# Performance work log

Hardware: AMD Instinct MI355X
Metric: run time of the kernel (lower is better)

Reference implementation:

```python
import jax, jax.numpy as jnp
import numpy as np

N_SCALES = 11
N_TAPS = 4
D4 = [0.4829629131445341, 0.8365163037378079, 0.2241438680420134, -0.1294095225512604]
B, N, D, H = 4, 2048, 1024, 16
HD = D // H  # 64


def setup_inputs() -> dict:
    key = jax.random.key(0)
    ks = jax.random.split(key, 8)
    s = 0.02
    return {
        "x": jax.random.normal(ks[0], (B, N, D), jnp.float32),
        "W_qkv": jax.random.normal(ks[1], (3 * D, D), jnp.float32) * s,
        "b_qkv": jnp.zeros((3 * D,), jnp.float32),
        "W_out": jax.random.normal(ks[2], (D, D), jnp.float32) * s,
        "b_out": jnp.zeros((D,), jnp.float32),
        "W_gate": jax.random.normal(ks[3], (D, D), jnp.float32) * s,
        "b_gate": jnp.full((D,), 2.0, jnp.float32),  # nn.init.constant_(gate bias, 2.0)
        "scale_gain": jax.random.normal(ks[4], (N_SCALES, H), jnp.float32) * 0.1,
        "W_qscale": jax.random.normal(ks[5], (N_SCALES, HD), jnp.float32) * 0.01,
        "identity_bypass": jnp.full((H,), -4.0, jnp.float32),
        "pos_bias": jax.random.normal(ks[6], (N_SCALES * N_TAPS, H), jnp.float32) * 0.01,
    }


def reference(x, W_qkv, b_qkv, W_out, b_out, W_gate, b_gate, scale_gain, W_qscale, identity_bypass, pos_bias):
    # qkv projection and head split -> [B,H,N,HD]
    qkv = x @ W_qkv.T + b_qkv
    q, k, v = jnp.split(qkv, 3, axis=-1)
    to_heads = lambda t: t.reshape(B, N, H, HD).transpose(0, 2, 1, 3)
    q, k, v = to_heads(q), to_heads(k), to_heads(v)

    # Q-conditioned per-scale gains: [B,H,N,n_scales]
    q_offset = jnp.einsum('bhnd,sd->bhns', q, W_qscale)
    prior = scale_gain.T[None, :, None, :]  # [1,H,1,S]
    gains = jax.nn.softmax(q_offset + prior, axis=-1)

    out = jnp.zeros((B, H, N, HD), q.dtype)
    z = jnp.zeros((B, H, N, 1), q.dtype)
    tap_idx = 0
    for j in range(N_SCALES):  # fixed small structural loop (44 taps total)
        d = 1 << j
        g_j = gains[..., j][..., None]  # [B,H,N,1]
        for tau, h_coef in enumerate(D4):
            offset = d * tau
            bias_jt = pos_bias[tap_idx].reshape(1, H, 1, 1)
            tap_idx += 1
            if offset != 0 and offset >= N:
                continue
            if offset == 0:
                k_s, v_s = k, v
            else:
                pad = jnp.zeros((B, H, offset, HD), k.dtype)
                k_s = jnp.concatenate([pad, k[:, :, :N - offset, :]], axis=2)
                v_s = jnp.concatenate([pad, v[:, :, :N - offset, :]], axis=2)
            qk_feat = jax.nn.elu(jnp.sum(q * k_s, -1, keepdims=True) + bias_jt) + 1.0
            out = out + (g_j * h_coef) * qk_feat * v_s
            z = z + g_j * abs(h_coef) * qk_feat

    # identity bypass (offset-0 local term)
    bypass = jax.nn.softplus(identity_bypass).reshape(1, H, 1, 1)
    local_ft = jax.nn.elu(jnp.sum(q * k, -1, keepdims=True)) + 1.0
    out = out + bypass * local_ft * v
    z = z + bypass * local_ft
    out = out / (z + 1e-06)

    gathered = out.transpose(0, 2, 1, 3).reshape(B, N, D)
    gate = jax.nn.sigmoid(x @ W_gate.T + b_gate)
    return (gathered * gate) @ W_out.T + b_out  # dropout p: eval mode -> identity
```

## Files before the change

kernel.cpp:

```cpp
#include <hip/hip_runtime.h>
#include <hip/hip_bf16.h>

#define PB 4
#define PN 2048
#define PD 1024
#define PH 16
#define PHD 64
#define NSC 11

typedef __attribute__((ext_vector_type(8))) short short8;
typedef __attribute__((ext_vector_type(4))) float floatx4;

#define AS1 __attribute__((address_space(1)))
#define AS3 __attribute__((address_space(3)))

static __device__ __forceinline__ unsigned short bf16bits(float f) {
    __hip_bfloat16 h = __float2bfloat16(f);
    return __builtin_bit_cast(unsigned short, h);
}

__global__ void cast_f32_to_bf16_v4(const float4* __restrict__ in,
                                    ushort4* __restrict__ out, int n4) {
    int i = blockIdx.x * blockDim.x + threadIdx.x;
    if (i < n4) {
        float4 v = in[i];
        ushort4 o;
        o.x = bf16bits(v.x);
        o.y = bf16bits(v.y);
        o.z = bf16bits(v.z);
        o.w = bf16bits(v.w);
        out[i] = o;
    }
}

#define GBM 128
#define GBN 128
#define GBK 64

template <int EPI>
__global__ __launch_bounds__(256) void gemm_bt128(
    const __hip_bfloat16* __restrict__ A,
    const __hip_bfloat16* __restrict__ Bm,
    const float* __restrict__ bias,
    const float* __restrict__ extra,
    void* __restrict__ outp,
    int Nn, int K) {
    __shared__ alignas(16) __hip_bfloat16 sA[GBM * GBK];
    __shared__ alignas(16) __hip_bfloat16 sB[GBN * GBK];

    const int tid = threadIdx.x;
    const int lane = tid & 63;
    const int wave = tid >> 6;
    const int wy = wave >> 1;
    const int wx = wave & 1;

    const int lrow8 = lane >> 3;
    const int lchunk = lane & 7;
    const int gchunk = lchunk ^ lrow8;

    const int r16 = lane & 15;
    const int qd = lane >> 4;
    const int sw = r16 & 7;

    floatx4 acc[4][4];
#pragma unroll
    for (int i = 0; i < 4; i++)
#pragma unroll
        for (int j = 0; j < 4; j++) acc[i][j] = (floatx4){0.f, 0.f, 0.f, 0.f};

    const size_t arow0 = (size_t)blockIdx.y * GBM;
    const size_t brow0 = (size_t)blockIdx.x * GBN;

    for (int k0 = 0; k0 < K; k0 += GBK) {
        __syncthreads();
#pragma unroll
        for (int half = 0; half < 4; half++) {
            const int rbase = wave * 8 + half * 32;
            const __hip_bfloat16* gA =
                A + (arow0 + rbase + lrow8) * K + k0 + gchunk * 8;
            __builtin_amdgcn_global_load_lds(
                (const AS1 unsigned int*)(const void*)gA,
                (AS3 unsigned int*)(void*)(sA + rbase * GBK), 16, 0, 0);
            const __hip_bfloat16* gB =
                Bm + (brow0 + rbase + lrow8) * K + k0 + gchunk * 8;
            __builtin_amdgcn_global_load_lds(
                (const AS1 unsigned int*)(const void*)gB,
                (AS3 unsigned int*)(void*)(sB + rbase * GBK), 16, 0, 0);
        }
        __syncthreads();

#pragma unroll
        for (int kk = 0; kk < 2; kk++) {
            short8 af[4], bf[4];
            const int cs = (qd + 4 * kk);
#pragma unroll
            for (int i = 0; i < 4; i++)
                af[i] = *(const short8*)(sA + (wy * 64 + i * 16 + r16) * GBK +
                                         ((cs ^ sw) * 8));
#pragma unroll
            for (int j = 0; j < 4; j++)
                bf[j] = *(const short8*)(sB + (wx * 64 + j * 16 + r16) * GBK +
                                         ((cs ^ sw) * 8));
#pragma unroll
            for (int i = 0; i < 4; i++)
#pragma unroll
                for (int j = 0; j < 4; j++)
                    acc[i][j] = __builtin_amdgcn_mfma_f32_16x16x32_bf16(
                        af[i], bf[j], acc[i][j], 0, 0, 0);
        }
    }

#pragma unroll
    for (int i = 0; i < 4; i++) {
#pragma unroll
        for (int j = 0; j < 4; j++) {
#pragma unroll
            for (int e = 0; e < 4; e++) {
                const size_t row = arow0 + wy * 64 + i * 16 + qd * 4 + e;
                const size_t col = brow0 + wx * 64 + j * 16 + r16;
                float v = acc[i][j][e] + bias[col];
                if (EPI == 0) {
                    ((float*)outp)[row * Nn + col] = v;
                } else {
                    float g = 1.f / (1.f + __expf(-v));
                    float a = extra[row * Nn + col];
                    ((__hip_bfloat16*)outp)[row * Nn + col] = __float2bfloat16(a * g);
                }
            }
        }
    }
}


__device__ __constant__ const int OFFS[21] = {1, 2, 3, 4, 6, 8, 12, 16, 24, 32, 48,
                                              64, 96, 128, 192, 256, 384, 512, 768, 1024, 1536};
__device__ __constant__ const int U1J[21] = {0, 0, 0, 1, 1, 2, 2, 3, 3, 4, 4,
                                             5, 5, 6, 6, 7, 7, 8, 8, 9, 9};
__device__ __constant__ const int U1T[21] = {1, 2, 3, 2, 3, 2, 3, 2, 3, 2, 3,
                                             2, 3, 2, 3, 2, 3, 2, 3, 2, 3};
__device__ __constant__ const int U2J[21] = {-1, 1, -1, 2, -1, 3, -1, 4, -1, 5, -1,
                                             6, -1, 7, -1, 8, -1, 9, -1, 10, -1};

static __device__ __forceinline__ float red16(float s) {
    int t;
    t = __builtin_amdgcn_update_dpp(0, __builtin_bit_cast(int, s), 0x121, 0xF, 0xF, true);
    s += __builtin_bit_cast(float, t);
    t = __builtin_amdgcn_update_dpp(0, __builtin_bit_cast(int, s), 0x122, 0xF, 0xF, true);
    s += __builtin_bit_cast(float, t);
    t = __builtin_amdgcn_update_dpp(0, __builtin_bit_cast(int, s), 0x124, 0xF, 0xF, true);
    s += __builtin_bit_cast(float, t);
    t = __builtin_amdgcn_update_dpp(0, __builtin_bit_cast(int, s), 0x128, 0xF, 0xF, true);
    s += __builtin_bit_cast(float, t);
    return s;
}

__global__ __launch_bounds__(256) void attn_kernel(
    const float* __restrict__ qkv,
    const float* __restrict__ scale_gain,
    const float* __restrict__ W_qscale,
    const float* __restrict__ identity_bypass,
    const float* __restrict__ pos_bias,
    float* __restrict__ att) {
    const int lane = threadIdx.x & 63;
    const int p = lane >> 4;
    const int l = lane & 15;

    const int flat = (blockIdx.x * 4 + (threadIdx.x >> 6)) * 4;
    const int n = (flat & (PN - 1)) + p;
    const int h = (flat >> 11) & (PH - 1);
    const int b = flat >> 15;

    const size_t base_bn = (size_t)b * PN;
    const int col = h * PHD + l * 4;

    const float4 q4 = *(const float4*)(qkv + (base_bn + n) * (3 * PD) + col);
    const float4 k04 = *(const float4*)(qkv + (base_bn + n) * (3 * PD) + PD + col);
    const float4 v04 = *(const float4*)(qkv + (base_bn + n) * (3 * PD) + 2 * PD + col);

    auto dot16 = [](float4 a, float4 b) {
        float s = a.x * b.x;
        s = fmaf(a.y, b.y, s);
        s = fmaf(a.z, b.z, s);
        s = fmaf(a.w, b.w, s);
        return red16(s);
    };

    const float dot0 = dot16(q4, k04);

    float g[NSC];
    float mx = -1e30f;
#pragma unroll
    for (int s = 0; s < NSC; s++) {
        const float4 w4 = *(const float4*)(W_qscale + s * PHD + l * 4);
        g[s] = dot16(q4, w4) + scale_gain[s * PH + h];
        mx = fmaxf(mx, g[s]);
    }
    float ssum = 0.f;
#pragma unroll
    for (int s = 0; s < NSC; s++) {
        g[s] = __expf(g[s] - mx);
        ssum += g[s];
    }
    const float inv = 1.f / ssum;
#pragma unroll
    for (int s = 0; s < NSC; s++) g[s] *= inv;

    const float D4c[4] = {0.4829629131445341f, 0.8365163037378079f,
                          0.2241438680420134f, -0.1294095225512604f};

    float4 out4 = {0.f, 0.f, 0.f, 0.f};
    float z = 0.f;

#pragma unroll
    for (int j = 0; j < NSC; j++) {
        const float xx = dot0 + pos_bias[(j * 4) * PH + h];
        const float feat = (xx > 0.f ? xx : __expf(xx) - 1.f) + 1.f;
        const float w = g[j] * D4c[0] * feat;
        out4.x = fmaf(w, v04.x, out4.x);
        out4.y = fmaf(w, v04.y, out4.y);
        out4.z = fmaf(w, v04.z, out4.z);
        out4.w = fmaf(w, v04.w, out4.w);
        z = fmaf(g[j] * D4c[0], feat, z);
    }

#pragma unroll
    for (int t = 0; t < 21; t++) {
        const int off = OFFS[t];
        const bool valid = (n >= off);
        const int idx = valid ? (n - off) : 0;
        const size_t rb = (base_bn + idx) * (3 * PD);
        float4 k4 = *(const float4*)(qkv + rb + PD + col);
        float4 v4 = *(const float4*)(qkv + rb + 2 * PD + col);
        const float vm = valid ? 1.f : 0.f;
        const float dv = dot16(q4, k4) * vm;
        v4.x *= vm; v4.y *= vm; v4.z *= vm; v4.w *= vm;

        {
            const int j = U1J[t], tau = U1T[t];
            const float xx = dv + pos_bias[(j * 4 + tau) * PH + h];
            const float feat = (xx > 0.f ? xx : __expf(xx) - 1.f) + 1.f;
            const float coef = D4c[tau];
            const float w = g[j] * coef * feat;
            out4.x = fmaf(w, v4.x, out4.x);
            out4.y = fmaf(w, v4.y, out4.y);
            out4.z = fmaf(w, v4.z, out4.z);
            out4.w = fmaf(w, v4.w, out4.w);
            z = fmaf(g[j] * fabsf(coef), feat, z);
        }
        if (U2J[t] >= 0) {
            const int j = U2J[t];
            const float xx = dv + pos_bias[(j * 4 + 1) * PH + h];
            const float feat = (xx > 0.f ? xx : __expf(xx) - 1.f) + 1.f;
            const float coef = D4c[1];
            const float w = g[j] * coef * feat;
            out4.x = fmaf(w, v4.x, out4.x);
            out4.y = fmaf(w, v4.y, out4.y);
            out4.z = fmaf(w, v4.z, out4.z);
            out4.w = fmaf(w, v4.w, out4.w);
            z = fmaf(g[j] * fabsf(coef), feat, z);
        }
    }

    const float bp = log1pf(__expf(identity_bypass[h]));
    const float f0 = (dot0 > 0.f ? dot0 : __expf(dot0) - 1.f) + 1.f;
    const float w0 = bp * f0;
    out4.x = fmaf(w0, v04.x, out4.x);
    out4.y = fmaf(w0, v04.y, out4.y);
    out4.z = fmaf(w0, v04.z, out4.z);
    out4.w = fmaf(w0, v04.w, out4.w);
    z += w0;

    const float zi = 1.f / (z + 1e-6f);
    float4 o;
    o.x = out4.x * zi; o.y = out4.y * zi; o.z = out4.z * zi; o.w = out4.w * zi;
    *(float4*)(att + (base_bn + n) * PD + col) = o;
}

extern "C" void kernel_launch(void* const* d_in, const int* in_sizes, int n_in,
                              void* d_out, int out_size, void* d_ws, size_t ws_size,
                              hipStream_t stream) {
    const float* x = (const float*)d_in[0];
    const float* W_qkv = (const float*)d_in[1];
    const float* b_qkv = (const float*)d_in[2];
    const float* W_out = (const float*)d_in[3];
    const float* b_out = (const float*)d_in[4];
    const float* W_gate = (const float*)d_in[5];
    const float* b_gate = (const float*)d_in[6];
    const float* scale_gain = (const float*)d_in[7];
    const float* W_qscale = (const float*)d_in[8];
    const float* identity_bypass = (const float*)d_in[9];
    const float* pos_bias = (const float*)d_in[10];
    float* out = (float*)d_out;

    const int M = PB * PN;
    char* ws = (char*)d_ws;
    size_t off = 0;
    auto alloc = [&](size_t bytes) -> void* {
        void* p = ws + off;
        off += (bytes + 255) & ~(size_t)255;
        return p;
    };
    __hip_bfloat16* x_bf = (__hip_bfloat16*)alloc((size_t)M * PD * 2);
    __hip_bfloat16* wqkv_bf = (__hip_bfloat16*)alloc((size_t)3 * PD * PD * 2);
    __hip_bfloat16* wgate_bf = (__hip_bfloat16*)alloc((size_t)PD * PD * 2);
    __hip_bfloat16* wout_bf = (__hip_bfloat16*)alloc((size_t)PD * PD * 2);
    float* qkv = (float*)alloc((size_t)M * 3 * PD * 4);
    float* att = (float*)alloc((size_t)M * PD * 4);
    __hip_bfloat16* gated = (__hip_bfloat16*)alloc((size_t)M * PD * 2);

    cast_f32_to_bf16_v4<<<(M * PD / 4) / 256, 256, 0, stream>>>(
        (const float4*)x, (ushort4*)x_bf, M * PD / 4);
    cast_f32_to_bf16_v4<<<(3 * PD * PD / 4) / 256, 256, 0, stream>>>(
        (const float4*)W_qkv, (ushort4*)wqkv_bf, 3 * PD * PD / 4);
    cast_f32_to_bf16_v4<<<(PD * PD / 4) / 256, 256, 0, stream>>>(
        (const float4*)W_gate, (ushort4*)wgate_bf, PD * PD / 4);
    cast_f32_to_bf16_v4<<<(PD * PD / 4) / 256, 256, 0, stream>>>(
        (const float4*)W_out, (ushort4*)wout_bf, PD * PD / 4);

    gemm_bt128<0><<<dim3(3 * PD / GBN, M / GBM), 256, 0, stream>>>(
        x_bf, wqkv_bf, b_qkv, nullptr, qkv, 3 * PD, PD);

    attn_kernel<<<(PB * PH * PN) / 16, 256, 0, stream>>>(
        qkv, scale_gain, W_qscale, identity_bypass, pos_bias, att);

    gemm_bt128<1><<<dim3(PD / GBN, M / GBM), 256, 0, stream>>>(
        x_bf, wgate_bf, b_gate, att, gated, PD, PD);

    gemm_bt128<0><<<dim3(PD / GBN, M / GBM), 256, 0, stream>>>(
        gated, wout_bf, b_out, nullptr, out, PD, PD);
}
```

Measured before the change: 340.9 us.

## Fuse gate projection into QKV GEMM and apply sigmoid gating in attention

Concatenates W_gate onto W_qkv so a single GEMM produces q, k, v and gate pre-activations into one 4*D-wide buffer. The attention kernel then reads the gate logits, applies the sigmoid, and writes the gated output directly as bf16. This removes the separate gate GEMM and the fp32 attention-output round trip. The three weight casts are also merged into one launch. In exchange, the qkv buffer row stride grows, which may hurt locality of the shifted k/v reads in the attention kernel.

```diff
diff --git a/kernel.cpp b/kernel.cpp
--- a/kernel.cpp
+++ b/kernel.cpp
@@ -33,17 +33,45 @@
     }
 }
 
+__global__ void cast_weights(const float4* __restrict__ wqkv,
+                             const float4* __restrict__ wgate,
+                             const float4* __restrict__ wout,
+                             ushort4* __restrict__ wcomb,
+                             ushort4* __restrict__ woutb) {
+    int i = blockIdx.x * blockDim.x + threadIdx.x;
+    const int QKV4 = 3 * PD * PD / 4;
+    const int G4 = PD * PD / 4;
+    float4 v;
+    ushort4* dst;
+    if (i < QKV4) {
+        v = wqkv[i];
+        dst = wcomb + i;
+    } else if (i < QKV4 + G4) {
+        v = wgate[i - QKV4];
+        dst = wcomb + i;
+    } else {
+        v = wout[i - QKV4 - G4];
+        dst = woutb + (i - QKV4 - G4);
+    }
+    ushort4 o;
+    o.x = bf16bits(v.x);
+    o.y = bf16bits(v.y);
+    o.z = bf16bits(v.z);
+    o.w = bf16bits(v.w);
+    *dst = o;
+}
+
 #define GBM 128
 #define GBN 128
 #define GBK 64
 
-template <int EPI>
 __global__ __launch_bounds__(256) void gemm_bt128(
     const __hip_bfloat16* __restrict__ A,
     const __hip_bfloat16* __restrict__ Bm,
-    const float* __restrict__ bias,
-    const float* __restrict__ extra,
-    void* __restrict__ outp,
+    const float* __restrict__ b1,
+    const float* __restrict__ b2,
+    int split,
+    float* __restrict__ outp,
     int Nn, int K) {
     __shared__ alignas(16) __hip_bfloat16 sA[GBM * GBK];
     __shared__ alignas(16) __hip_bfloat16 sB[GBN * GBK];
@@ -114,23 +142,18 @@
     for (int i = 0; i < 4; i++) {
 #pragma unroll
         for (int j = 0; j < 4; j++) {
+            const int colb = (int)brow0 + wx * 64 + j * 16 + r16;
+            const float bb = (colb < split) ? b1[colb] : b2[colb - split];
 #pragma unroll
             for (int e = 0; e < 4; e++) {
                 const size_t row = arow0 + wy * 64 + i * 16 + qd * 4 + e;
-                const size_t col = brow0 + wx * 64 + j * 16 + r16;
-                float v = acc[i][j][e] + bias[col];
-                if (EPI == 0) {
-                    ((float*)outp)[row * Nn + col] = v;
-                } else {
-                    float g = 1.f / (1.f + __expf(-v));
-                    float a = extra[row * Nn + col];
-                    ((__hip_bfloat16*)outp)[row * Nn + col] = __float2bfloat16(a * g);
-                }
+                outp[row * Nn + colb] = acc[i][j][e] + bb;
             }
         }
     }
 }
 
+#define RS (4 * PD)
 
 __device__ __constant__ const int OFFS[21] = {1, 2, 3, 4, 6, 8, 12, 16, 24, 32, 48,
                                               64, 96, 128, 192, 256, 384, 512, 768, 1024, 1536};
@@ -155,17 +178,19 @@
 }
 
 __global__ __launch_bounds__(256) void attn_kernel(
-    const float* __restrict__ qkv,
+    const float* __restrict__ qkvg,
     const float* __restrict__ scale_gain,
     const float* __restrict__ W_qscale,
     const float* __restrict__ identity_bypass,
     const float* __restrict__ pos_bias,
-    float* __restrict__ att) {
+    __hip_bfloat16* __restrict__ gated) {
     const int lane = threadIdx.x & 63;
     const int p = lane >> 4;
     const int l = lane & 15;
 
-    const int flat = (blockIdx.x * 4 + (threadIdx.x >> 6)) * 4;
+    const int wid =
+        __builtin_amdgcn_readfirstlane(blockIdx.x * 4 + (threadIdx.x >> 6));
+    const int flat = wid * 4;
     const int n = (flat & (PN - 1)) + p;
     const int h = (flat >> 11) & (PH - 1);
     const int b = flat >> 15;
@@ -173,9 +198,11 @@
     const size_t base_bn = (size_t)b * PN;
     const int col = h * PHD + l * 4;
 
-    const float4 q4 = *(const float4*)(qkv + (base_bn + n) * (3 * PD) + col);
-    const float4 k04 = *(const float4*)(qkv + (base_bn + n) * (3 * PD) + PD + col);
-    const float4 v04 = *(const float4*)(qkv + (base_bn + n) * (3 * PD) + 2 * PD + col);
+    const float* row0 = qkvg + (base_bn + n) * RS + col;
+    const float4 q4 = *(const float4*)row0;
+    const float4 k04 = *(const float4*)(row0 + PD);
+    const float4 v04 = *(const float4*)(row0 + 2 * PD);
+    const float4 gp4 = *(const float4*)(row0 + 3 * PD);
 
     auto dot16 = [](float4 a, float4 b) {
         float s = a.x * b.x;
@@ -228,9 +255,9 @@
         const int off = OFFS[t];
         const bool valid = (n >= off);
         const int idx = valid ? (n - off) : 0;
-        const size_t rb = (base_bn + idx) * (3 * PD);
-        float4 k4 = *(const float4*)(qkv + rb + PD + col);
-        float4 v4 = *(const float4*)(qkv + rb + 2 * PD + col);
+        const float* rowk = qkvg + (base_bn + idx) * RS + PD + col;
+        float4 k4 = *(const float4*)rowk;
+        float4 v4 = *(const float4*)(rowk + PD);
         const float vm = valid ? 1.f : 0.f;
         const float dv = dot16(q4, k4) * vm;
         v4.x *= vm; v4.y *= vm; v4.z *= vm; v4.w *= vm;
@@ -271,9 +298,12 @@
     z += w0;
 
     const float zi = 1.f / (z + 1e-6f);
-    float4 o;
-    o.x = out4.x * zi; o.y = out4.y * zi; o.z = out4.z * zi; o.w = out4.w * zi;
-    *(float4*)(att + (base_bn + n) * PD + col) = o;
+    ushort4 o;
+    o.x = bf16bits(out4.x * zi / (1.f + __expf(-gp4.x)));
+    o.y = bf16bits(out4.y * zi / (1.f + __expf(-gp4.y)));
+    o.z = bf16bits(out4.z * zi / (1.f + __expf(-gp4.z)));
+    o.w = bf16bits(out4.w * zi / (1.f + __expf(-gp4.w)));
+    *(ushort4*)(gated + (base_bn + n) * PD + col) = o;
 }
 
 extern "C" void kernel_launch(void* const* d_in, const int* in_sizes, int n_in,
@@ -301,31 +331,23 @@
         return p;
     };
     __hip_bfloat16* x_bf = (__hip_bfloat16*)alloc((size_t)M * PD * 2);
-    __hip_bfloat16* wqkv_bf = (__hip_bfloat16*)alloc((size_t)3 * PD * PD * 2);
-    __hip_bfloat16* wgate_bf = (__hip_bfloat16*)alloc((size_t)PD * PD * 2);
+    __hip_bfloat16* wcomb_bf = (__hip_bfloat16*)alloc((size_t)4 * PD * PD * 2);
     __hip_bfloat16* wout_bf = (__hip_bfloat16*)alloc((size_t)PD * PD * 2);
-    float* qkv = (float*)alloc((size_t)M * 3 * PD * 4);
-    float* att = (float*)alloc((size_t)M * PD * 4);
+    float* qkvg = (float*)alloc((size_t)M * 4 * PD * 4);
     __hip_bfloat16* gated = (__hip_bfloat16*)alloc((size_t)M * PD * 2);
 
     cast_f32_to_bf16_v4<<<(M * PD / 4) / 256, 256, 0, stream>>>(
         (const float4*)x, (ushort4*)x_bf, M * PD / 4);
-    cast_f32_to_bf16_v4<<<(3 * PD * PD / 4) / 256, 256, 0, stream>>>(
-        (const float4*)W_qkv, (ushort4*)wqkv_bf, 3 * PD * PD / 4);
-    cast_f32_to_bf16_v4<<<(PD * PD / 4) / 256, 256, 0, stream>>>(
-        (const float4*)W_gate, (ushort4*)wgate_bf, PD * PD / 4);
-    cast_f32_to_bf16_v4<<<(PD * PD / 4) / 256, 256, 0, stream>>>(
-        (const float4*)W_out, (ushort4*)wout_bf, PD * PD / 4);
-
-    gemm_bt128<0><<<dim3(3 * PD / GBN, M / GBM), 256, 0, stream>>>(
-        x_bf, wqkv_bf, b_qkv, nullptr, qkv, 3 * PD, PD);
+    cast_weights<<<(5 * PD * PD / 4) / 256, 256, 0, stream>>>(
+        (const float4*)W_qkv, (const float4*)W_gate, (const float4*)W_out,
+        (ushort4*)wcomb_bf, (ushort4*)wout_bf);
+
+    gemm_bt128<<<dim3(4 * PD / GBN, M / GBM), 256, 0, stream>>>(
+        x_bf, wcomb_bf, b_qkv, b_gate, 3 * PD, qkvg, 4 * PD, PD);
 
     attn_kernel<<<(PB * PH * PN) / 16, 256, 0, stream>>>(
-        qkv, scale_gain, W_qscale, identity_bypass, pos_bias, att);
-
-    gemm_bt128<1><<<dim3(PD / GBN, M / GBM), 256, 0, stream>>>(
-        x_bf, wgate_bf, b_gate, att, gated, PD, PD);
-
-    gemm_bt128<0><<<dim3(PD / GBN, M / GBM), 256, 0, stream>>>(
-        gated, wout_bf, b_out, nullptr, out, PD, PD);
-}
+        qkvg, scale_gain, W_qscale, identity_bypass, pos_bias, gated);
+
+    gemm_bt128<<<dim3(PD / GBN, M / GBM), 256, 0, stream>>>(
+        gated, wout_bf, b_out, b_out, PD, out, PD, PD);
+}
```

Result: slower. 381.4 us (+11.9%).
